# Kernel optimization log

Measured on AMD Instinct MI355X. Metric: run time of the kernel, lower is better.

Reference implementation:

```python
import jax, jax.numpy as jnp
import numpy as np

NUM_PIECES = 32

def _conv(x, w, pad):
    # NCHW conv, stride 1
    return jax.lax.conv_general_dilated(x, w, (1, 1), [(pad, pad), (pad, pad)],
                                        dimension_numbers=('NCHW', 'OIHW', 'NCHW'))

def _bn(x, s, b):
    # eval-mode BatchNorm folded to per-channel affine (running mean/var folded into s,b)
    return x * s[None, :, None, None] + b[None, :, None, None]

def setup_inputs() -> dict:
    key = jax.random.key(0)
    ks = jax.random.split(key, 24)
    N, CIN, H, W = 1024, 13, 8, 8
    C = 64          # final conv channels
    S, NB = 7, 7    # stages, conv blocks per stage
    P = NUM_PIECES
    feat = jax.random.normal(ks[0], (N, CIN - 1, H, W), jnp.float32)
    ids = jax.random.randint(ks[1], (N, 1, H, W), 0, P + 1).astype(jnp.float32)
    x = jnp.concatenate([feat, ids], axis=1)  # last channel = piece ids
    n = jax.random.normal
    inp = {
        'x': x,
        'first_w': n(ks[2], (C - 1, CIN - 1, 7, 7), jnp.float32) * 0.05,
        'first_s': 1.0 + 0.1 * n(ks[3], (C - 1,), jnp.float32),
        'first_b': 0.05 * n(ks[4], (C - 1,), jnp.float32),
        'res_w': n(ks[5], (S, NB, C, C, 7, 7), jnp.float32) * 0.02,
        'res_s': 1.0 + 0.1 * n(ks[6], (S, NB, C), jnp.float32),
        'res_b': 0.05 * n(ks[7], (S, NB, C), jnp.float32),
        'last_w': n(ks[8], (S, C, C), jnp.float32) * 0.05,
        'last_s': 1.0 + 0.1 * n(ks[9], (S, C), jnp.float32),
        'last_b': 0.05 * n(ks[10], (S, C), jnp.float32),
        'pfc1_w': n(ks[11], (256, P * C), jnp.float32) * 0.02,
        'pfc1_b': jnp.zeros((256,), jnp.float32),
        'pfc2_w': n(ks[12], (1700, 256), jnp.float32) * 0.02,
        'pfc2_b': jnp.zeros((1700,), jnp.float32),
        'vconv_w': n(ks[13], (1, C, 1, 1), jnp.float32) * 0.05,
        'v_s': 1.0 + 0.1 * n(ks[14], (1,), jnp.float32),
        'v_b': 0.05 * n(ks[15], (1,), jnp.float32),
        'vfc1_w': n(ks[16], (256, H * W), jnp.float32) * 0.02,
        'vfc1_b': jnp.zeros((256,), jnp.float32),
        'vfc2_w': n(ks[17], (1, 256), jnp.float32) * 0.02,
        'vfc2_b': jnp.zeros((1,), jnp.float32),
    }
    return inp

def reference(x, first_w, first_s, first_b, res_w, res_s, res_b, last_w, last_s, last_b,
              pfc1_w, pfc1_b, pfc2_w, pfc2_b, vconv_w, v_s, v_b,
              vfc1_w, vfc1_b, vfc2_w, vfc2_b):
    N = x.shape[0]
    P = NUM_PIECES
    conv_in = x[:, :-1]           # (N, 12, 8, 8)
    ids_f = x[:, -1]              # (N, 8, 8) float piece ids
    ids = ids_f.astype(jnp.int32)
    h = jax.nn.relu(_bn(_conv(conv_in, first_w, 3), first_s, first_b))  # (N, 63, 8, 8)
    conv_feat = jnp.concatenate([h, ids_f[:, None]], axis=1)            # (N, 64, 8, 8)
    # --- fused piece-vector extraction (replaces batch x piece torch.where loop) ---
    ids_flat = ids.reshape(N, -1)                                       # (N, 64)
    match = ids_flat[:, None, :] == jnp.arange(1, P + 1, dtype=jnp.int32)[None, :, None]  # (N,P,64)
    idx = jnp.argmax(match, axis=-1)                                    # first occurrence, row-major
    present = match.any(-1)
    board_t = conv_feat.reshape(N, conv_feat.shape[1], -1).transpose(0, 2, 1)  # (N, 64pos, C)
    piece_vec = jnp.take_along_axis(board_t, idx[:, :, None], axis=1)          # (N, P, C)
    piece_vec = piece_vec * present[:, :, None].astype(piece_vec.dtype)
    pid_hist = [piece_vec[:, :, -1][:, None, :]]
    S, NB = res_w.shape[0], res_w.shape[1]
    for i in range(S):
        h = conv_feat
        for j in range(NB):
            h = jax.nn.relu(_bn(_conv(h, res_w[i, j], 3), res_s[i, j], res_b[i, j]))
        h = _bn(jnp.einsum('nchw,oc->nohw', h, last_w[i]), last_s[i], last_b[i])  # 1x1 conv
        conv_feat = jax.nn.relu(h + conv_feat)
        pid_hist.append(piece_vec[:, :, -1][:, None, :])
    piece_ids_out = jnp.concatenate(pid_hist, axis=1)  # (N, S+1, P)
    # policy head
    hid = jax.nn.relu(piece_vec.reshape(N, -1) @ pfc1_w.T + pfc1_b)
    policy = hid @ pfc2_w.T + pfc2_b                   # (N, 1700)
    # value head
    v = jax.nn.relu(_bn(_conv(conv_feat, vconv_w, 0), v_s, v_b)).reshape(N, -1)  # (N, 64)
    v = jax.nn.relu(v @ vfc1_w.T + vfc1_b)
    value = jnp.tanh(v @ vfc2_w.T + vfc2_b)            # (N, 1)
    return (policy, value, piece_ids_out)
```

## Files before the change

### kernel.cpp

```cpp
#include <hip/hip_runtime.h>

typedef __attribute__((ext_vector_type(8)))  short          bf16x8;
typedef __attribute__((ext_vector_type(16))) float          f32x16;
typedef __attribute__((ext_vector_type(8)))  unsigned int   u32x8;
typedef __attribute__((ext_vector_type(4)))  unsigned short ushort4v;
typedef __attribute__((ext_vector_type(4)))  float          float4v;

#define DEV static __device__ __forceinline__
#define MFMA32(A,B,C) __builtin_amdgcn_mfma_f32_32x32x16_bf16(A,B,C,0,0,0)

#define NTILES   2408
#define WRES_OFF 0u
#define FW_OFF   9863168u
#define P1_OFF   9913344u
#define P2_OFF   10437632u
#define ACT0_OFF 10896384u
#define PV_OFF   15090688u
#define HID_OFF  17187840u

#define VAL_OFF 1740800
#define PID_OFF 1741824

#define SM_Z     32768
#define WBUF_OFF 32896
#define SM_BYTES 57472

DEV float bf2f(unsigned short u){ union { unsigned int i; float f; } v; v.i = ((unsigned int)u) << 16; return v.f; }
DEV unsigned short f2bf(float f){
  union { float f; unsigned int i; } v; v.f = f;
  unsigned int x = v.i;
  return (unsigned short)((x + 0x7fffu + ((x >> 16) & 1u)) >> 16);
}

__global__ void prep_res_k(const float* __restrict__ res_w, unsigned short* __restrict__ ws){
  __shared__ float buf[3136];
  int bx = blockIdx.x;
  int L = bx >> 6, o = bx & 63;
  const float* src = res_w + (size_t)bx * 3136;
  for (int e = threadIdx.x; e < 3136; e += 256) buf[e] = src[e];
  __syncthreads();
  unsigned short* dst = ws + WRES_OFF;
  int mt = o >> 5, lrow = o & 31;
  int tilebase = L*49 + L/7;
  for (int e = threadIdx.x; e < 3136; e += 256){
    int t = e >> 6, c = e & 63;
    int ks = c >> 4, hi = (c >> 3) & 1, j = c & 7;
    int lane = hi*32 + lrow;
    dst[(size_t)(tilebase + t)*4096 + ((ks*2 + mt)*64 + lane)*8 + j] = f2bf(buf[c*49 + t]);
  }
}

__global__ void prep_misc_k(const float* __restrict__ first_w, const float* __restrict__ last_w,
                            const float* __restrict__ pfc1_w, const float* __restrict__ pfc2_w,
                            unsigned short* __restrict__ ws){
  const int n_fw = 49*1024, n_lw = 28672, n_p1 = 524288, n_p2 = 458752;
  const int total = n_fw + n_lw + n_p1 + n_p2;
  for (int d = blockIdx.x*256 + threadIdx.x; d < total; d += gridDim.x*256){
    if (d < n_fw){
      int t = d >> 10, r = d & 1023;
      int mt = r >> 9, lane = (r >> 3) & 63, j = r & 7;
      int o = mt*32 + (lane & 31);
      int c = ((lane >> 5) << 3) + j;
      float v = (o < 63 && c < 12) ? first_w[(o*12 + c)*49 + t] : 0.f;
      ws[FW_OFF + d] = f2bf(v);
    } else if (d < n_fw + n_lw){
      int e = d - n_fw;
      int st = e >> 12, r = e & 4095;
      int f = r >> 9, lane = (r >> 3) & 63, j = r & 7;
      int ks = f >> 1, mt = f & 1;
      int o = mt*32 + (lane & 31);
      int c = ks*16 + ((lane >> 5) << 3) + j;
      ws[WRES_OFF + (size_t)(st*344 + 343)*4096 + r] = f2bf(last_w[st*4096 + o*64 + c]);
    } else if (d < n_fw + n_lw + n_p1){
      int e = d - n_fw - n_lw; ws[P1_OFF + e] = f2bf(pfc1_w[e]);
    } else {
      int e = d - n_fw - n_lw - n_p1;
      int row = e >> 8, k = e & 255;
      ws[P2_OFF + e] = f2bf(row < 1700 ? pfc2_w[row*256 + k] : 0.f);
    }
  }
}

DEV int baddr(int q, bool valid, int imgbase, int hi){
  int sz = (q & 7) << 4;
  int a = (q << 7) + ((imgbase + hi*16) ^ sz);
  return valid ? a : (SM_Z + hi*16);
}

DEV void stage_tile(unsigned char* sm, const unsigned short* wstream, int s, int wave, int lane){
  const unsigned short* g = wstream + (size_t)s*4096 + wave*512 + lane*8;
  unsigned char* l = sm + WBUF_OFF + (s % 3)*8192 + wave*1024;
  __builtin_amdgcn_global_load_lds((const __attribute__((address_space(1))) unsigned int*)g,
                                   (__attribute__((address_space(3))) unsigned int*)l, 16, 0, 0);
}

DEV void conv_epi(const f32x16& acc, int mt, int p, int imgbase, int hi,
                  unsigned char* smp, const float* sp, const float* bp){
  int swzw = (p & 7) << 4; int rowb = imgbase + (p << 7);
  #pragma unroll
  for (int rg = 0; rg < 4; ++rg){
    int o0 = mt*32 + rg*8 + hi*4;
    unsigned short bb[4];
    #pragma unroll
    for (int e = 0; e < 4; ++e){
      float v = sp[o0+e]*acc[rg*4+e] + bp[o0+e];
      v = v > 0.f ? v : 0.f;
      bb[e] = f2bf(v);
    }
    int ob = mt*64 + rg*16 + hi*8;
    *(ushort4v*)(smp + rowb + (ob ^ swzw)) = ushort4v{bb[0],bb[1],bb[2],bb[3]};
  }
}

DEV void res_epi(const f32x16& acc, u32x8& res, int mt, int p, int imgbase, int hi,
                 unsigned char* smp, const float* lsp, const float* lbp){
  int swzw = (p & 7) << 4; int rowb = imgbase + (p << 7);
  #pragma unroll
  for (int rg = 0; rg < 4; ++rg){
    int o0 = mt*32 + rg*8 + hi*4;
    unsigned short bb[4];
    #pragma unroll
    for (int e = 0; e < 4; ++e){
      unsigned pr = res[rg*2 + (e>>1)];
      float rv = bf2f((unsigned short)((e & 1) ? (pr >> 16) : (pr & 0xffffu)));
      float v = lsp[o0+e]*acc[rg*4+e] + lbp[o0+e] + rv;
      v = v > 0.f ? v : 0.f;
      bb[e] = f2bf(v);
    }
    res[rg*2]   = (unsigned)bb[0] | ((unsigned)bb[1] << 16);
    res[rg*2+1] = (unsigned)bb[2] | ((unsigned)bb[3] << 16);
    int ob = mt*64 + rg*16 + hi*8;
    *(ushort4v*)(smp + rowb + (ob ^ swzw)) = ushort4v{bb[0],bb[1],bb[2],bb[3]};
  }
}

DEV void first_epi(const f32x16& acc, u32x8& res, int mt, int p, float idsv,
                   int img, int imgbase, int hi, unsigned char* smp,
                   const float* fsp, const float* fbp, unsigned short* act0){
  int swzw = (p & 7) << 4; int rowb = imgbase + (p << 7);
  #pragma unroll
  for (int rg = 0; rg < 4; ++rg){
    int o0 = mt*32 + rg*8 + hi*4;
    unsigned short bb[4];
    #pragma unroll
    for (int e = 0; e < 4; ++e){
      int o = o0 + e;
      int oc = o < 63 ? o : 62;
      float v = fsp[oc]*acc[rg*4+e] + fbp[oc];
      v = v > 0.f ? v : 0.f;
      if (o == 63) v = idsv;
      bb[e] = f2bf(v);
    }
    res[rg*2]   = (unsigned)bb[0] | ((unsigned)bb[1] << 16);
    res[rg*2+1] = (unsigned)bb[2] | ((unsigned)bb[3] << 16);
    int ob = mt*64 + rg*16 + hi*8;
    *(ushort4v*)(smp + rowb + (ob ^ swzw)) = ushort4v{bb[0],bb[1],bb[2],bb[3]};
    *(ushort4v*)(act0 + (size_t)img*4096 + p*64 + o0) = ushort4v{bb[0],bb[1],bb[2],bb[3]};
  }
}

__global__ __launch_bounds__(512, 1) void tower_k(
    const float* __restrict__ x,
    const float* __restrict__ first_s, const float* __restrict__ first_b,
    const float* __restrict__ res_s,   const float* __restrict__ res_b,
    const float* __restrict__ last_s,  const float* __restrict__ last_b,
    const float* __restrict__ vconv_w, const float* __restrict__ v_s, const float* __restrict__ v_b,
    const float* __restrict__ vfc1_w,  const float* __restrict__ vfc1_b,
    const float* __restrict__ vfc2_w,  const float* __restrict__ vfc2_b,
    const unsigned short* ws_r, unsigned short* act0, float* value_out)
{
  __shared__ unsigned char sm[SM_BYTES];
  int tid = threadIdx.x, lane = tid & 63, wave = tid >> 6;
  int imgi = wave & 3, sub = wave >> 2;
  int img = blockIdx.x * 4 + imgi;

  for (int i = tid*16; i < SM_BYTES; i += 512*16) *(float4v*)(sm + i) = float4v{0,0,0,0};
  __syncthreads();

  int col = lane & 31, hi = lane >> 5;
  int imgbase = imgi * 8192;
  int xinbase = WBUF_OFF + imgi * 3584;

  int p0 = col, p1 = 32 + col;
  int y0 = p0 >> 3, x0v = p0 & 7, y1 = p1 >> 3, x1v = p1 & 7;

  const unsigned short* wstream = ws_r + WRES_OFF;
  const float* xim = x + (size_t)img * 832;
  if (sub == 0){
    int q = (lane >> 3)*14 + (lane & 7) + 3;
    for (int c = 0; c < 12; ++c)
      *(unsigned short*)(sm + xinbase + q*32 + c*2) = f2bf(xim[c*64 + lane]);
  }
  float ids0 = xim[768 + p0];
  float ids1 = xim[768 + p1];
  __syncthreads();

  f32x16 f0 = {}, f1 = {};
  const unsigned short* fw = ws_r + FW_OFF;
  int qb0x = y0*14 + x0v, qb1x = y1*14 + x1v;
  #pragma unroll
  for (int dy = 0; dy < 7; ++dy){
    bool v0 = (unsigned)(y0 + dy - 3) < 8u;
    bool v1 = (unsigned)(y1 + dy - 3) < 8u;
    int tq = (dy-3)*14;
    #pragma unroll
    for (int dx = 0; dx < 7; ++dx){
      int t = dy*7 + dx;
      bf16x8 a = *(const bf16x8*)(fw + t*1024 + sub*512 + lane*8);
      int q0 = qb0x + tq + dx, q1 = qb1x + tq + dx;
      int b0a = v0 ? (xinbase + q0*32 + hi*16) : (SM_Z + hi*16);
      int b1a = v1 ? (xinbase + q1*32 + hi*16) : (SM_Z + hi*16);
      bf16x8 bb0 = *(const bf16x8*)(sm + b0a);
      bf16x8 bb1 = *(const bf16x8*)(sm + b1a);
      f0 = MFMA32(a, bb0, f0);
      f1 = MFMA32(a, bb1, f1);
    }
  }
  u32x8 res0, res1;
  first_epi(f0, res0, sub, p0, ids0, img, imgbase, hi, sm, first_s, first_b, act0);
  first_epi(f1, res1, sub, p1, ids1, img, imgbase, hi, sm, first_s, first_b, act0);
  __syncthreads();

  stage_tile(sm, wstream, 0, wave, lane);
  stage_tile(sm, wstream, 1, wave, lane);

  f32x16 c0 = {}, c1 = {};
  int dy = 0, dx = 0, L = 0, st = 0;
  for (int s = 0; s < NTILES; ++s){
    if (s + 2 < NTILES) stage_tile(sm, wstream, s + 2, wave, lane);
    if (s < NTILES - 2)       asm volatile("s_waitcnt vmcnt(2)" ::: "memory");
    else if (s == NTILES - 2) asm volatile("s_waitcnt vmcnt(1)" ::: "memory");
    else                      asm volatile("s_waitcnt vmcnt(0)" ::: "memory");
    __builtin_amdgcn_s_barrier();
    asm volatile("" ::: "memory");
    const unsigned short* wb = (const unsigned short*)(sm + WBUF_OFF + (s % 3)*8192);
    int r = s - st*344;
    if (r < 343){
      bool v0 = ((unsigned)(y0 + dy - 3) < 8u) && ((unsigned)(x0v + dx - 3) < 8u);
      bool v1 = ((unsigned)(y1 + dy - 3) < 8u) && ((unsigned)(x1v + dx - 3) < 8u);
      int off = (dy - 3)*8 + (dx - 3);
      bf16x8 ak[4];
      #pragma unroll
      for (int ks = 0; ks < 4; ++ks)
        ak[ks] = *(const bf16x8*)(wb + (ks*2 + sub)*512 + lane*8);
      int b0 = baddr(p0 + off, v0, imgbase, hi);
      int b1 = baddr(p1 + off, v1, imgbase, hi);
      #pragma unroll
      for (int ks = 0; ks < 4; ++ks){
        bf16x8 bf0 = *(const bf16x8*)(sm + (b0 ^ (ks << 5)));
        bf16x8 bf1 = *(const bf16x8*)(sm + (b1 ^ (ks << 5)));
        c0 = MFMA32(ak[ks], bf0, c0);
        c1 = MFMA32(ak[ks], bf1, c1);
      }
      ++dx;
      if (dx == 7){ dx = 0; ++dy; }
      if (dy == 7){
        dy = 0;
        const float* sp = res_s + L*64;
        const float* bp = res_b + L*64;
        conv_epi(c0, sub, p0, imgbase, hi, sm, sp, bp);
        conv_epi(c1, sub, p1, imgbase, hi, sm, sp, bp);
        c0 = f32x16{}; c1 = f32x16{};
        ++L;
      }
    } else {
      const float* lsp = last_s + st*64;
      const float* lbp = last_b + st*64;
      f32x16 d0 = {}, d1 = {};
      int bA = baddr(p0, true, imgbase, hi);
      int bB = baddr(p1, true, imgbase, hi);
      #pragma unroll
      for (int ks = 0; ks < 4; ++ks){
        bf16x8 a  = *(const bf16x8*)(wb + (ks*2 + sub)*512 + lane*8);
        bf16x8 b0 = *(const bf16x8*)(sm + (bA ^ (ks << 5)));
        bf16x8 b1 = *(const bf16x8*)(sm + (bB ^ (ks << 5)));
        d0 = MFMA32(a, b0, d0);
        d1 = MFMA32(a, b1, d1);
      }
      res_epi(d0, res0, sub, p0, imgbase, hi, sm, lsp, lbp);
      res_epi(d1, res1, sub, p1, imgbase, hi, sm, lsp, lbp);
      ++st;
    }
    asm volatile("s_waitcnt lgkmcnt(0)" ::: "memory");
    __builtin_amdgcn_s_barrier();
    asm volatile("" ::: "memory");
  }

  float part0 = 0.f, part1 = 0.f;
  #pragma unroll
  for (int rg = 0; rg < 4; ++rg){
    #pragma unroll
    for (int eh = 0; eh < 2; ++eh){
      unsigned pA0 = res0[rg*2+eh], pA1 = res1[rg*2+eh];
      int ob = sub*32 + rg*8 + hi*4 + eh*2;
      float w0 = vconv_w[ob], w1 = vconv_w[ob+1];
      part0 += bf2f((unsigned short)(pA0 & 0xffffu))*w0 + bf2f((unsigned short)(pA0 >> 16))*w1;
      part1 += bf2f((unsigned short)(pA1 & 0xffffu))*w0 + bf2f((unsigned short)(pA1 >> 16))*w1;
    }
  }
  part0 += __shfl_xor(part0, 32);
  part1 += __shfl_xor(part1, 32);
  float* vp = (float*)(sm + WBUF_OFF);
  float pv = hi ? part1 : part0;
  vp[(imgi*2 + sub)*64 + hi*32 + col] = pv;
  __syncthreads();

  if (wave < 4){
    int mimg = blockIdx.x*4 + wave;
    float vs = v_s[0], vb = v_b[0];
    float sum = vp[(wave*2)*64 + lane] + vp[(wave*2 + 1)*64 + lane];
    float vv = vs*sum + vb; vv = vv > 0.f ? vv : 0.f;
    float* vbuf = (float*)(sm + WBUF_OFF + 2048) + wave*64;
    vbuf[lane] = vv;
    float hidv[4];
    #pragma unroll
    for (int it = 0; it < 4; ++it){
      int jj = it*64 + lane;
      float a = vfc1_b[jj];
      for (int k = 0; k < 64; k += 4){
        float4v vv4 = *(const float4v*)(vbuf + k);
        a += vfc1_w[jj*64+k]*vv4[0] + vfc1_w[jj*64+k+1]*vv4[1]
           + vfc1_w[jj*64+k+2]*vv4[2] + vfc1_w[jj*64+k+3]*vv4[3];
      }
      hidv[it] = a > 0.f ? a : 0.f;
    }
    float tot = 0.f;
    #pragma unroll
    for (int it = 0; it < 4; ++it) tot += hidv[it]*vfc2_w[it*64 + lane];
    #pragma unroll
    for (int off = 32; off; off >>= 1) tot += __shfl_xor(tot, off);
    if (lane == 0) value_out[mimg] = tanhf(tot + vfc2_b[0]);
  }
}

__global__ __launch_bounds__(256) void gather_k(const unsigned short* __restrict__ act0,
                                                unsigned short* __restrict__ pvec,
                                                float* __restrict__ pid_out){
  int lane = threadIdx.x & 63, wave = threadIdx.x >> 6;
  int img = blockIdx.x*4 + wave;
  const unsigned short* arow = act0 + (size_t)img*4096;
  int myid = (int)bf2f(arow[lane*64 + 63]);
  int mypos = 0, mypres = 0;
  for (int p = 0; p < 32; ++p){
    unsigned long long m = __ballot(myid == (p+1));
    if (lane == p){ mypres = (m != 0ull); mypos = mypres ? (__ffsll(m) - 1) : 0; }
  }
  if (lane < 32){
    float v = mypres ? (float)(lane+1) : 0.f;
    #pragma unroll
    for (int s = 0; s < 8; ++s) pid_out[(size_t)img*256 + s*32 + lane] = v;
  }
  for (int p = 0; p < 32; ++p){
    int q  = __shfl(mypos, p);
    int pr = __shfl(mypres, p);
    unsigned short v = pr ? arow[q*64 + lane] : (unsigned short)0;
    pvec[(size_t)img*2048 + p*64 + lane] = v;
  }
}

__global__ __launch_bounds__(256) void fc1_k(const unsigned short* __restrict__ pvec,
                                             const unsigned short* __restrict__ w,
                                             const float* __restrict__ bias,
                                             unsigned short* __restrict__ hid){
  int lane = threadIdx.x & 63, wave = threadIdx.x >> 6;
  int col = lane & 31, hi = lane >> 5;
  int wm = wave >> 1, wn = wave & 1;
  int m0 = blockIdx.x*128 + wm*64;
  int n0 = blockIdx.y*128 + wn*64;
  f32x16 a00 = {}, a01 = {}, a10 = {}, a11 = {};
  for (int k = 0; k < 2048; k += 16){
    bf16x8 A0 = *(const bf16x8*)(pvec + (size_t)(m0+col)*2048    + k + hi*8);
    bf16x8 A1 = *(const bf16x8*)(pvec + (size_t)(m0+32+col)*2048 + k + hi*8);
    bf16x8 B0 = *(const bf16x8*)(w + (size_t)(n0+col)*2048    + k + hi*8);
    bf16x8 B1 = *(const bf16x8*)(w + (size_t)(n0+32+col)*2048 + k + hi*8);
    a00 = MFMA32(A0, B0, a00); a01 = MFMA32(A0, B1, a01);
    a10 = MFMA32(A1, B0, a10); a11 = MFMA32(A1, B1, a11);
  }
  #pragma unroll
  for (int mt = 0; mt < 2; ++mt)
    #pragma unroll
    for (int nt = 0; nt < 2; ++nt){
      const f32x16& acc = mt == 0 ? (nt == 0 ? a00 : a01) : (nt == 0 ? a10 : a11);
      int jcol = n0 + nt*32 + col;
      float bj = bias[jcol];
      #pragma unroll
      for (int rg = 0; rg < 4; ++rg)
        #pragma unroll
        for (int e = 0; e < 4; ++e){
          int n = m0 + mt*32 + rg*8 + hi*4 + e;
          float v = acc[rg*4+e] + bj; v = v > 0.f ? v : 0.f;
          hid[(size_t)n*256 + jcol] = f2bf(v);
        }
    }
}

__global__ __launch_bounds__(256) void fc2_k(const unsigned short* __restrict__ hid,
                                             const unsigned short* __restrict__ w,
                                             const float* __restrict__ bias,
                                             float* __restrict__ pol){
  int lane = threadIdx.x & 63, wave = threadIdx.x >> 6;
  int col = lane & 31, hi = lane >> 5;
  int wm = wave >> 1, wn = wave & 1;
  int m0 = blockIdx.x*128 + wm*64;
  int n0 = blockIdx.y*128 + wn*64;
  f32x16 a00 = {}, a01 = {}, a10 = {}, a11 = {};
  for (int k = 0; k < 256; k += 16){
    bf16x8 A0 = *(const bf16x8*)(hid + (size_t)(m0+col)*256    + k + hi*8);
    bf16x8 A1 = *(const bf16x8*)(hid + (size_t)(m0+32+col)*256 + k + hi*8);
    bf16x8 B0 = *(const bf16x8*)(w + (size_t)(n0+col)*256    + k + hi*8);
    bf16x8 B1 = *(const bf16x8*)(w + (size_t)(n0+32+col)*256 + k + hi*8);
    a00 = MFMA32(A0, B0, a00); a01 = MFMA32(A0, B1, a01);
    a10 = MFMA32(A1, B0, a10); a11 = MFMA32(A1, B1, a11);
  }
  #pragma unroll
  for (int mt = 0; mt < 2; ++mt)
    #pragma unroll
    for (int nt = 0; nt < 2; ++nt){
      const f32x16& acc = mt == 0 ? (nt == 0 ? a00 : a01) : (nt == 0 ? a10 : a11);
      int jcol = n0 + nt*32 + col;
      if (jcol < 1700){
        float bj = bias[jcol];
        #pragma unroll
        for (int rg = 0; rg < 4; ++rg)
          #pragma unroll
          for (int e = 0; e < 4; ++e){
            int n = m0 + mt*32 + rg*8 + hi*4 + e;
            pol[(size_t)n*1700 + jcol] = acc[rg*4+e] + bj;
          }
      }
    }
}

extern "C" void kernel_launch(void* const* d_in, const int* in_sizes, int n_in,
                              void* d_out, int out_size, void* d_ws, size_t ws_size,
                              hipStream_t stream){
  const float* x       = (const float*)d_in[0];
  const float* first_w = (const float*)d_in[1];
  const float* first_s = (const float*)d_in[2];
  const float* first_b = (const float*)d_in[3];
  const float* res_w   = (const float*)d_in[4];
  const float* res_s   = (const float*)d_in[5];
  const float* res_b   = (const float*)d_in[6];
  const float* last_w  = (const float*)d_in[7];
  const float* last_s  = (const float*)d_in[8];
  const float* last_b  = (const float*)d_in[9];
  const float* pfc1_w  = (const float*)d_in[10];
  const float* pfc1_b  = (const float*)d_in[11];
  const float* pfc2_w  = (const float*)d_in[12];
  const float* pfc2_b  = (const float*)d_in[13];
  const float* vconv_w = (const float*)d_in[14];
  const float* v_s     = (const float*)d_in[15];
  const float* v_b     = (const float*)d_in[16];
  const float* vfc1_w  = (const float*)d_in[17];
  const float* vfc1_b  = (const float*)d_in[18];
  const float* vfc2_w  = (const float*)d_in[19];
  const float* vfc2_b  = (const float*)d_in[20];
  unsigned short* ws = (unsigned short*)d_ws;
  float* out = (float*)d_out;

  prep_res_k <<<3136, 256, 0, stream>>>(res_w, ws);
  prep_misc_k<<<1024, 256, 0, stream>>>(first_w, last_w, pfc1_w, pfc2_w, ws);
  tower_k    <<<256, 512, 0, stream>>>(x, first_s, first_b, res_s, res_b, last_s, last_b,
                                       vconv_w, v_s, v_b, vfc1_w, vfc1_b, vfc2_w, vfc2_b,
                                       ws, ws + ACT0_OFF, out + VAL_OFF);
  gather_k   <<<256, 256, 0, stream>>>(ws + ACT0_OFF, ws + PV_OFF, out + PID_OFF);
  fc1_k      <<<dim3(8, 2), 256, 0, stream>>>(ws + PV_OFF, ws + P1_OFF, pfc1_b, ws + HID_OFF);
  fc2_k      <<<dim3(8, 14), 256, 0, stream>>>(ws + HID_OFF, ws + P2_OFF, pfc2_b, out);
}
```

Baseline: 1.701 ms.

## Restructure tower kernel: 1024 threads, direct weight loads, ping-pong activations

The tower kernel now runs 16 waves per block, each computing one 32-position group for one 32-channel half of one image, where it previously used 8 waves each handling two position groups. Weights now come from global memory (cache) straight into registers, double-buffered across taps. This replaces the per-tap global_load_lds staging into a triple LDS buffer, which needed two barriers per tap. Activations ping-pong between two LDS buffers, so only one barrier per layer is needed. The aim is to remove per-tap synchronisation and raise parallelism, at the cost of more redundant weight traffic through L1/L2 and of register pressure at 1024 threads.

```diff
diff --git a/kernel.cpp b/kernel.cpp
--- a/kernel.cpp
+++ b/kernel.cpp
@@ -21,9 +21,10 @@
 #define VAL_OFF 1740800
 #define PID_OFF 1741824
 
-#define SM_Z     32768
-#define WBUF_OFF 32896
-#define SM_BYTES 57472
+#define ACT_A    0
+#define ACT_B    32768
+#define SM_Z     65536
+#define SM_BYTES 65792
 
 DEV float bf2f(unsigned short u){ union { unsigned int i; float f; } v; v.i = ((unsigned int)u) << 16; return v.f; }
 DEV unsigned short f2bf(float f){
@@ -81,25 +82,32 @@
   }
 }
 
-DEV int baddr(int q, bool valid, int imgbase, int hi){
-  int sz = (q & 7) << 4;
-  int a = (q << 7) + ((imgbase + hi*16) ^ sz);
-  return valid ? a : (SM_Z + hi*16);
-}
-
-DEV void stage_tile(unsigned char* sm, const unsigned short* wstream, int s, int wave, int lane){
-  const unsigned short* g = wstream + (size_t)s*4096 + wave*512 + lane*8;
-  unsigned char* l = sm + WBUF_OFF + (s % 3)*8192 + wave*1024;
-  __builtin_amdgcn_global_load_lds((const __attribute__((address_space(1))) unsigned int*)g,
-                                   (__attribute__((address_space(3))) unsigned int*)l, 16, 0, 0);
-}
-
-DEV void conv_epi(const f32x16& acc, int mt, int p, int imgbase, int hi,
+
+#define LOADW(W, q) { \
+  W[0] = *(const bf16x8*)(q); \
+  W[1] = *(const bf16x8*)((q) + 1024); \
+  W[2] = *(const bf16x8*)((q) + 2048); \
+  W[3] = *(const bf16x8*)((q) + 3072); }
+
+#define TAPB(W, dyc, dxc) { \
+  bool v_ = ((unsigned)(py + (dyc) - 3) < 8u) && ((unsigned)(px + (dxc) - 3) < 8u); \
+  int pp_ = p + ((dyc) - 3)*8 + ((dxc) - 3); \
+  int b_ = v_ ? (rbase + (pp_ << 7) + (hi16 ^ ((pp_ & 7) << 4))) : zaddr; \
+  c0 = MFMA32(W[0], *(const bf16x8*)(sm + b_),        c0); \
+  c0 = MFMA32(W[1], *(const bf16x8*)(sm + (b_ ^ 32)), c0); \
+  c0 = MFMA32(W[2], *(const bf16x8*)(sm + (b_ ^ 64)), c0); \
+  c0 = MFMA32(W[3], *(const bf16x8*)(sm + (b_ ^ 96)), c0); }
+
+#define LBAR() { asm volatile("s_waitcnt lgkmcnt(0)" ::: "memory"); \
+                 __builtin_amdgcn_s_barrier(); \
+                 asm volatile("" ::: "memory"); }
+
+DEV void conv_epi(const f32x16& acc, int sub, int p, int wrow, int hi,
                   unsigned char* smp, const float* sp, const float* bp){
-  int swzw = (p & 7) << 4; int rowb = imgbase + (p << 7);
+  int swzw = (p & 7) << 4;
   #pragma unroll
   for (int rg = 0; rg < 4; ++rg){
-    int o0 = mt*32 + rg*8 + hi*4;
+    int o0 = sub*32 + rg*8 + hi*4;
     unsigned short bb[4];
     #pragma unroll
     for (int e = 0; e < 4; ++e){
@@ -107,17 +115,17 @@
       v = v > 0.f ? v : 0.f;
       bb[e] = f2bf(v);
     }
-    int ob = mt*64 + rg*16 + hi*8;
-    *(ushort4v*)(smp + rowb + (ob ^ swzw)) = ushort4v{bb[0],bb[1],bb[2],bb[3]};
-  }
-}
-
-DEV void res_epi(const f32x16& acc, u32x8& res, int mt, int p, int imgbase, int hi,
+    int ob = sub*64 + rg*16 + hi*8;
+    *(ushort4v*)(smp + wrow + (ob ^ swzw)) = ushort4v{bb[0],bb[1],bb[2],bb[3]};
+  }
+}
+
+DEV void res_epi(const f32x16& acc, u32x8& res, int sub, int p, int wrow, int hi,
                  unsigned char* smp, const float* lsp, const float* lbp){
-  int swzw = (p & 7) << 4; int rowb = imgbase + (p << 7);
+  int swzw = (p & 7) << 4;
   #pragma unroll
   for (int rg = 0; rg < 4; ++rg){
-    int o0 = mt*32 + rg*8 + hi*4;
+    int o0 = sub*32 + rg*8 + hi*4;
     unsigned short bb[4];
     #pragma unroll
     for (int e = 0; e < 4; ++e){
@@ -129,18 +137,18 @@
     }
     res[rg*2]   = (unsigned)bb[0] | ((unsigned)bb[1] << 16);
     res[rg*2+1] = (unsigned)bb[2] | ((unsigned)bb[3] << 16);
-    int ob = mt*64 + rg*16 + hi*8;
-    *(ushort4v*)(smp + rowb + (ob ^ swzw)) = ushort4v{bb[0],bb[1],bb[2],bb[3]};
-  }
-}
-
-DEV void first_epi(const f32x16& acc, u32x8& res, int mt, int p, float idsv,
-                   int img, int imgbase, int hi, unsigned char* smp,
+    int ob = sub*64 + rg*16 + hi*8;
+    *(ushort4v*)(smp + wrow + (ob ^ swzw)) = ushort4v{bb[0],bb[1],bb[2],bb[3]};
+  }
+}
+
+DEV void first_epi(const f32x16& acc, u32x8& res, int sub, int p, float idsv,
+                   int img, int wrow, int hi, unsigned char* smp,
                    const float* fsp, const float* fbp, unsigned short* act0){
-  int swzw = (p & 7) << 4; int rowb = imgbase + (p << 7);
+  int swzw = (p & 7) << 4;
   #pragma unroll
   for (int rg = 0; rg < 4; ++rg){
-    int o0 = mt*32 + rg*8 + hi*4;
+    int o0 = sub*32 + rg*8 + hi*4;
     unsigned short bb[4];
     #pragma unroll
     for (int e = 0; e < 4; ++e){
@@ -153,13 +161,13 @@
     }
     res[rg*2]   = (unsigned)bb[0] | ((unsigned)bb[1] << 16);
     res[rg*2+1] = (unsigned)bb[2] | ((unsigned)bb[3] << 16);
-    int ob = mt*64 + rg*16 + hi*8;
-    *(ushort4v*)(smp + rowb + (ob ^ swzw)) = ushort4v{bb[0],bb[1],bb[2],bb[3]};
+    int ob = sub*64 + rg*16 + hi*8;
+    *(ushort4v*)(smp + wrow + (ob ^ swzw)) = ushort4v{bb[0],bb[1],bb[2],bb[3]};
     *(ushort4v*)(act0 + (size_t)img*4096 + p*64 + o0) = ushort4v{bb[0],bb[1],bb[2],bb[3]};
   }
 }
 
-__global__ __launch_bounds__(512, 1) void tower_k(
+__global__ __launch_bounds__(1024, 4) void tower_k(
     const float* __restrict__ x,
     const float* __restrict__ first_s, const float* __restrict__ first_b,
     const float* __restrict__ res_s,   const float* __restrict__ res_b,
@@ -167,151 +175,119 @@
     const float* __restrict__ vconv_w, const float* __restrict__ v_s, const float* __restrict__ v_b,
     const float* __restrict__ vfc1_w,  const float* __restrict__ vfc1_b,
     const float* __restrict__ vfc2_w,  const float* __restrict__ vfc2_b,
-    const unsigned short* ws_r, unsigned short* act0, float* value_out)
+    const unsigned short* __restrict__ ws_r, unsigned short* __restrict__ act0,
+    float* __restrict__ value_out)
 {
   __shared__ unsigned char sm[SM_BYTES];
   int tid = threadIdx.x, lane = tid & 63, wave = tid >> 6;
-  int imgi = wave & 3, sub = wave >> 2;
+  int imgi = wave & 3, sub = (wave >> 2) & 1, pg = wave >> 3;
   int img = blockIdx.x * 4 + imgi;
 
-  for (int i = tid*16; i < SM_BYTES; i += 512*16) *(float4v*)(sm + i) = float4v{0,0,0,0};
+  for (int i = tid*16; i < SM_BYTES; i += 1024*16) *(float4v*)(sm + i) = float4v{0,0,0,0};
   __syncthreads();
 
   int col = lane & 31, hi = lane >> 5;
-  int imgbase = imgi * 8192;
-  int xinbase = WBUF_OFF + imgi * 3584;
-
-  int p0 = col, p1 = 32 + col;
-  int y0 = p0 >> 3, x0v = p0 & 7, y1 = p1 >> 3, x1v = p1 & 7;
-
-  const unsigned short* wstream = ws_r + WRES_OFF;
+  int hi16 = hi << 4;
+  int zaddr = SM_Z + hi16;
+  int p  = pg*32 + col;
+  int py = p >> 3, px = p & 7;
+
   const float* xim = x + (size_t)img * 832;
-  if (sub == 0){
+  int xinbase = ACT_B + imgi * 3584;
+  if (wave < 4){
     int q = (lane >> 3)*14 + (lane & 7) + 3;
     for (int c = 0; c < 12; ++c)
       *(unsigned short*)(sm + xinbase + q*32 + c*2) = f2bf(xim[c*64 + lane]);
   }
-  float ids0 = xim[768 + p0];
-  float ids1 = xim[768 + p1];
+  float idsv = xim[768 + p];
   __syncthreads();
 
-  f32x16 f0 = {}, f1 = {};
+  f32x16 f0 = {};
   const unsigned short* fw = ws_r + FW_OFF;
-  int qb0x = y0*14 + x0v, qb1x = y1*14 + x1v;
+  int qbx = py*14 + px;
   #pragma unroll
   for (int dy = 0; dy < 7; ++dy){
-    bool v0 = (unsigned)(y0 + dy - 3) < 8u;
-    bool v1 = (unsigned)(y1 + dy - 3) < 8u;
+    bool vy = (unsigned)(py + dy - 3) < 8u;
     int tq = (dy-3)*14;
     #pragma unroll
     for (int dx = 0; dx < 7; ++dx){
       int t = dy*7 + dx;
       bf16x8 a = *(const bf16x8*)(fw + t*1024 + sub*512 + lane*8);
-      int q0 = qb0x + tq + dx, q1 = qb1x + tq + dx;
-      int b0a = v0 ? (xinbase + q0*32 + hi*16) : (SM_Z + hi*16);
-      int b1a = v1 ? (xinbase + q1*32 + hi*16) : (SM_Z + hi*16);
-      bf16x8 bb0 = *(const bf16x8*)(sm + b0a);
-      bf16x8 bb1 = *(const bf16x8*)(sm + b1a);
-      f0 = MFMA32(a, bb0, f0);
-      f1 = MFMA32(a, bb1, f1);
-    }
-  }
-  u32x8 res0, res1;
-  first_epi(f0, res0, sub, p0, ids0, img, imgbase, hi, sm, first_s, first_b, act0);
-  first_epi(f1, res1, sub, p1, ids1, img, imgbase, hi, sm, first_s, first_b, act0);
+      int q0 = qbx + tq + dx;
+      int ba = vy ? (xinbase + q0*32 + hi16) : zaddr;
+      f0 = MFMA32(a, *(const bf16x8*)(sm + ba), f0);
+    }
+  }
+  u32x8 res0;
+  first_epi(f0, res0, sub, p, idsv, img, ACT_A + imgi*8192 + (p << 7), hi, sm,
+            first_s, first_b, act0);
   __syncthreads();
 
-  stage_tile(sm, wstream, 0, wave, lane);
-  stage_tile(sm, wstream, 1, wave, lane);
-
-  f32x16 c0 = {}, c1 = {};
-  int dy = 0, dx = 0, L = 0, st = 0;
-  for (int s = 0; s < NTILES; ++s){
-    if (s + 2 < NTILES) stage_tile(sm, wstream, s + 2, wave, lane);
-    if (s < NTILES - 2)       asm volatile("s_waitcnt vmcnt(2)" ::: "memory");
-    else if (s == NTILES - 2) asm volatile("s_waitcnt vmcnt(1)" ::: "memory");
-    else                      asm volatile("s_waitcnt vmcnt(0)" ::: "memory");
-    __builtin_amdgcn_s_barrier();
-    asm volatile("" ::: "memory");
-    const unsigned short* wb = (const unsigned short*)(sm + WBUF_OFF + (s % 3)*8192);
-    int r = s - st*344;
-    if (r < 343){
-      bool v0 = ((unsigned)(y0 + dy - 3) < 8u) && ((unsigned)(x0v + dx - 3) < 8u);
-      bool v1 = ((unsigned)(y1 + dy - 3) < 8u) && ((unsigned)(x1v + dx - 3) < 8u);
-      int off = (dy - 3)*8 + (dx - 3);
-      bf16x8 ak[4];
+  int rbase = ACT_A + imgi*8192;
+  int wbase = ACT_B + imgi*8192;
+  const unsigned short* gw = ws_r + WRES_OFF + sub*512 + lane*8;
+
+  for (int st = 0; st < 7; ++st){
+    for (int j = 0; j < 7; ++j){
+      int L = st*7 + j;
+      f32x16 c0 = {};
+      bf16x8 wA[4], wB[4];
+      LOADW(wA, gw);
       #pragma unroll
-      for (int ks = 0; ks < 4; ++ks)
-        ak[ks] = *(const bf16x8*)(wb + (ks*2 + sub)*512 + lane*8);
-      int b0 = baddr(p0 + off, v0, imgbase, hi);
-      int b1 = baddr(p1 + off, v1, imgbase, hi);
-      #pragma unroll
-      for (int ks = 0; ks < 4; ++ks){
-        bf16x8 bf0 = *(const bf16x8*)(sm + (b0 ^ (ks << 5)));
-        bf16x8 bf1 = *(const bf16x8*)(sm + (b1 ^ (ks << 5)));
-        c0 = MFMA32(ak[ks], bf0, c0);
-        c1 = MFMA32(ak[ks], bf1, c1);
+      for (int t = 0; t < 49; ++t){
+        const int dy = t / 7, dx = t % 7;
+        if ((t & 1) == 0){
+          if (t + 1 < 49) LOADW(wB, gw + (t+1)*4096);
+          TAPB(wA, dy, dx);
+        } else {
+          if (t + 1 < 49) LOADW(wA, gw + (t+1)*4096);
+          TAPB(wB, dy, dx);
+        }
       }
-      ++dx;
-      if (dx == 7){ dx = 0; ++dy; }
-      if (dy == 7){
-        dy = 0;
-        const float* sp = res_s + L*64;
-        const float* bp = res_b + L*64;
-        conv_epi(c0, sub, p0, imgbase, hi, sm, sp, bp);
-        conv_epi(c1, sub, p1, imgbase, hi, sm, sp, bp);
-        c0 = f32x16{}; c1 = f32x16{};
-        ++L;
-      }
-    } else {
-      const float* lsp = last_s + st*64;
-      const float* lbp = last_b + st*64;
-      f32x16 d0 = {}, d1 = {};
-      int bA = baddr(p0, true, imgbase, hi);
-      int bB = baddr(p1, true, imgbase, hi);
-      #pragma unroll
-      for (int ks = 0; ks < 4; ++ks){
-        bf16x8 a  = *(const bf16x8*)(wb + (ks*2 + sub)*512 + lane*8);
-        bf16x8 b0 = *(const bf16x8*)(sm + (bA ^ (ks << 5)));
-        bf16x8 b1 = *(const bf16x8*)(sm + (bB ^ (ks << 5)));
-        d0 = MFMA32(a, b0, d0);
-        d1 = MFMA32(a, b1, d1);
-      }
-      res_epi(d0, res0, sub, p0, imgbase, hi, sm, lsp, lbp);
-      res_epi(d1, res1, sub, p1, imgbase, hi, sm, lsp, lbp);
-      ++st;
-    }
-    asm volatile("s_waitcnt lgkmcnt(0)" ::: "memory");
-    __builtin_amdgcn_s_barrier();
-    asm volatile("" ::: "memory");
-  }
-
-  float part0 = 0.f, part1 = 0.f;
+      gw += 49*4096;
+      conv_epi(c0, sub, p, wbase + (p << 7), hi, sm, res_s + L*64, res_b + L*64);
+      LBAR();
+      int tmpb = rbase; rbase = wbase; wbase = tmpb;
+    }
+    {
+      bf16x8 wA[4];
+      LOADW(wA, gw); gw += 4096;
+      f32x16 d0 = {};
+      int b = rbase + (p << 7) + (hi16 ^ ((p & 7) << 4));
+      d0 = MFMA32(wA[0], *(const bf16x8*)(sm + b),        d0);
+      d0 = MFMA32(wA[1], *(const bf16x8*)(sm + (b ^ 32)), d0);
+      d0 = MFMA32(wA[2], *(const bf16x8*)(sm + (b ^ 64)), d0);
+      d0 = MFMA32(wA[3], *(const bf16x8*)(sm + (b ^ 96)), d0);
+      res_epi(d0, res0, sub, p, wbase + (p << 7), hi, sm, last_s + st*64, last_b + st*64);
+      LBAR();
+      int tmpb = rbase; rbase = wbase; wbase = tmpb;
+    }
+  }
+
+  float part = 0.f;
   #pragma unroll
   for (int rg = 0; rg < 4; ++rg){
     #pragma unroll
     for (int eh = 0; eh < 2; ++eh){
-      unsigned pA0 = res0[rg*2+eh], pA1 = res1[rg*2+eh];
+      unsigned pr = res0[rg*2+eh];
       int ob = sub*32 + rg*8 + hi*4 + eh*2;
-      float w0 = vconv_w[ob], w1 = vconv_w[ob+1];
-      part0 += bf2f((unsigned short)(pA0 & 0xffffu))*w0 + bf2f((unsigned short)(pA0 >> 16))*w1;
-      part1 += bf2f((unsigned short)(pA1 & 0xffffu))*w0 + bf2f((unsigned short)(pA1 >> 16))*w1;
-    }
-  }
-  part0 += __shfl_xor(part0, 32);
-  part1 += __shfl_xor(part1, 32);
-  float* vp = (float*)(sm + WBUF_OFF);
-  float pv = hi ? part1 : part0;
-  vp[(imgi*2 + sub)*64 + hi*32 + col] = pv;
+      part += bf2f((unsigned short)(pr & 0xffffu))*vconv_w[ob]
+            + bf2f((unsigned short)(pr >> 16))*vconv_w[ob+1];
+    }
+  }
+  part += __shfl_xor(part, 32);
+  float* vpf = (float*)(sm + ACT_B);
+  if (lane < 32) vpf[(imgi*2 + sub)*64 + pg*32 + lane] = part;
   __syncthreads();
 
   if (wave < 4){
     int mimg = blockIdx.x*4 + wave;
     float vs = v_s[0], vb = v_b[0];
-    float sum = vp[(wave*2)*64 + lane] + vp[(wave*2 + 1)*64 + lane];
+    float sum = vpf[(wave*2)*64 + lane] + vpf[(wave*2 + 1)*64 + lane];
     float vv = vs*sum + vb; vv = vv > 0.f ? vv : 0.f;
-    float* vbuf = (float*)(sm + WBUF_OFF + 2048) + wave*64;
+    float* vbuf = (float*)(sm + ACT_B + 2048) + wave*64;
     vbuf[lane] = vv;
+    asm volatile("s_waitcnt lgkmcnt(0)" ::: "memory");
     float hidv[4];
     #pragma unroll
     for (int it = 0; it < 4; ++it){
@@ -460,9 +436,9 @@
 
   prep_res_k <<<3136, 256, 0, stream>>>(res_w, ws);
   prep_misc_k<<<1024, 256, 0, stream>>>(first_w, last_w, pfc1_w, pfc2_w, ws);
-  tower_k    <<<256, 512, 0, stream>>>(x, first_s, first_b, res_s, res_b, last_s, last_b,
-                                       vconv_w, v_s, v_b, vfc1_w, vfc1_b, vfc2_w, vfc2_b,
-                                       ws, ws + ACT0_OFF, out + VAL_OFF);
+  tower_k    <<<256, 1024, 0, stream>>>(x, first_s, first_b, res_s, res_b, last_s, last_b,
+                                        vconv_w, v_s, v_b, vfc1_w, vfc1_b, vfc2_w, vfc2_b,
+                                        ws, ws + ACT0_OFF, out + VAL_OFF);
   gather_k   <<<256, 256, 0, stream>>>(ws + ACT0_OFF, ws + PV_OFF, out + PID_OFF);
   fc1_k      <<<dim3(8, 2), 256, 0, stream>>>(ws + PV_OFF, ws + P1_OFF, pfc1_b, ws + HID_OFF);
   fc2_k      <<<dim3(8, 14), 256, 0, stream>>>(ws + HID_OFF, ws + P2_OFF, pfc2_b, out);
```

Measured after the change: 1.399 ms. 1.22x faster.
